# Performance work log

Measured on AMD Instinct MI355X. Metric: run time of the kernel, lower is better.

The kernel has to match this reference:

```python
import jax, jax.numpy as jnp
import numpy as np

B, D, H, K = 128, 512, 512, 16


def setup_inputs() -> dict:
    key = jax.random.key(0)
    ks = jax.random.split(key, 10)
    def xav(k, shape, fan_in, fan_out):
        # xavier_uniform per expert slice (same bound for all slices of the bank)
        bound = np.sqrt(6.0 / (fan_in + fan_out)).astype(np.float32)
        return jax.random.uniform(k, shape, jnp.float32, -bound, bound)
    u = jax.random.uniform(ks[9], (B, K), jnp.float32)
    u = u / jnp.sum(u, axis=-1, keepdims=True)  # soft convex selector
    return {
        "x_t": jax.random.normal(ks[0], (B, D), jnp.float32),
        "h_prev": jax.random.normal(ks[1], (B, H), jnp.float32),
        "u_t": u,
        "Wxr": xav(ks[2], (K, H, D), D, H),
        "Wxz": xav(ks[3], (K, H, D), D, H),
        "Wxn": xav(ks[4], (K, H, D), D, H),
        "Whr": xav(ks[5], (K, H, H), H, H),
        "Whz": xav(ks[6], (K, H, H), H, H),
        "Whn": xav(ks[7], (K, H, H), H, H),
        "bxr": jnp.zeros((K, H), jnp.float32),
        "bxz": jnp.zeros((K, H), jnp.float32),
        "bxn": jnp.zeros((K, H), jnp.float32),
        "brh": jnp.zeros((K, H), jnp.float32),
        "bzh": jnp.zeros((K, H), jnp.float32),
        "bnh": jnp.zeros((K, H), jnp.float32),
    }


def reference(x_t, h_prev, u_t, Wxr, Wxz, Wxn, Whr, Whz, Whn,
              bxr, bxz, bxn, brh, bzh, bnh):
    # mix biases: sum_k u[b,k] * b[k,h]
    mixb = lambda b: jnp.einsum('kh,bk->bh', b, u_t)
    # x-path: sum_k u[b,k] * (W[k] @ x[b]) + mixed bias; contracted without
    # materializing the [B,H,D] mixed weight (same math, better memory).
    def aff_x(W, b):
        return jnp.einsum('khd,bk,bd->bh', W, u_t, x_t, optimize=True) + mixb(b)
    # h-path: the original uses torch.einsum('bhh,bh->bh', W_mixed, h), which
    # extracts the DIAGONAL of the mixed [B,H,H] weight and multiplies
    # elementwise with h. Reproduce exactly via diagonals of the expert banks.
    def aff_h(W, b):
        dW = jnp.diagonal(W, axis1=1, axis2=2)  # [K, H]
        return jnp.einsum('kh,bk->bh', dW, u_t) * h_prev + mixb(b)
    r_t = jax.nn.sigmoid(aff_x(Wxr, bxr) + aff_h(Whr, brh))
    z_t = jax.nn.sigmoid(aff_x(Wxz, bxz) + aff_h(Whz, bzh))
    n_t = jnp.tanh(aff_x(Wxn, bxn) + r_t * aff_h(Whn, bnh))
    h_t = (1.0 - z_t) * n_t + z_t * h_prev
    return h_t
```

## Files before the change

kernel.cpp:

```cpp
#include <hip/hip_runtime.h>
#include <cstdint>
#include <cstddef>

#define Bb 128
#define Dd 512
#define Hh 512
#define KE 16

typedef unsigned short u16;
typedef unsigned int u32;
typedef __bf16 bf16x8 __attribute__((ext_vector_type(8)));
typedef float f32x4 __attribute__((ext_vector_type(4)));

union U8 { u16 h[8]; uint4 v; };

__device__ __forceinline__ u16 f2bf(float f) {
  u32 u = __float_as_uint(f);
  u32 r = (u + 0x7fffu + ((u >> 16) & 1u)) >> 16;
  return (u16)r;
}

__global__ __launch_bounds__(256) void prep_kernel(
    const float* __restrict__ x, const float* __restrict__ u,
    const float* __restrict__ Whr, const float* __restrict__ Whz,
    const float* __restrict__ Whn,
    u16* __restrict__ xu, float* __restrict__ yx, float* __restrict__ dW)
{
  int t = blockIdx.x * 256 + threadIdx.x;
  if (t < 131072) {
    int d8 = t & 63;
    int rest = t >> 6;
    int b = rest & 127;
    int k = rest >> 7;
    float uk = u[b * KE + k];
    const float4* xp = (const float4*)(x + b * Dd + d8 * 8);
    float4 x0 = xp[0], x1 = xp[1];
    U8 o;
    o.h[0] = f2bf(uk * x0.x); o.h[1] = f2bf(uk * x0.y);
    o.h[2] = f2bf(uk * x0.z); o.h[3] = f2bf(uk * x0.w);
    o.h[4] = f2bf(uk * x1.x); o.h[5] = f2bf(uk * x1.y);
    o.h[6] = f2bf(uk * x1.z); o.h[7] = f2bf(uk * x1.w);
    *(uint4*)(xu + ((k * Bb + b) * Dd + d8 * 8)) = o.v;
  } else if (t < 131072 + 49152) {
    int i = t - 131072;
    ((float4*)yx)[i] = make_float4(0.f, 0.f, 0.f, 0.f);
  } else if (t < 131072 + 49152 + 24576) {
    int i = t - (131072 + 49152);
    int h = i & 511;
    int k = (i >> 9) & 15;
    int bank = i >> 13;
    const float* Wp = bank == 0 ? Whr : (bank == 1 ? Whz : Whn);
    dW[i] = Wp[(size_t)k * Hh * Hh + h * (Hh + 1)];
  }
}

__global__ __launch_bounds__(256) void gemm_kernel(
    const float* __restrict__ Wxr, const float* __restrict__ Wxz,
    const float* __restrict__ Wxn,
    const u16* __restrict__ xu, float* __restrict__ yx)
{
  int bid = blockIdx.x;
  int k = bid & 15;
  int rem = bid >> 4;
  int bank = rem % 3;
  int ht = rem / 3;

  const float* Wsrc = (bank == 0 ? Wxr : (bank == 1 ? Wxz : Wxn));
  const float* Wp = Wsrc + (size_t)k * Hh * Dd + (size_t)ht * 128 * Dd;
  const u16* Ap = xu + k * Bb * Dd;
  float* yp = yx + bank * Bb * Hh;

  __shared__ __align__(16) u16 lA[2][128 * 64];
  __shared__ __align__(16) u16 lB[2][128 * 64];

  int tid = threadIdx.x;
  int lane = tid & 63;
  int wave = tid >> 6;
  int wm = wave >> 1;
  int wn = wave & 1;

  int ar = tid >> 1;
  int ac = (tid & 1) * 32;
  int br = tid >> 2;
  int bc = (tid & 3) * 16;

  uint4 aL[4];
  float4 bL[2][4];

  f32x4 acc[4][4];
#pragma unroll
  for (int i = 0; i < 4; ++i)
#pragma unroll
    for (int j = 0; j < 4; ++j) acc[i][j] = (f32x4){0.f, 0.f, 0.f, 0.f};

  auto LOAD = [&](int c) {
    int d0 = c * 64;
#pragma unroll
    for (int q = 0; q < 4; ++q)
      aL[q] = *(const uint4*)(Ap + ar * Dd + d0 + ac + 8 * q);
#pragma unroll
    for (int p = 0; p < 2; ++p)
#pragma unroll
      for (int q = 0; q < 4; ++q)
        bL[p][q] = *(const float4*)(Wp + (br + 64 * p) * Dd + d0 + bc + 4 * q);
  };

  auto STORE = [&](int nb) {
#pragma unroll
    for (int q = 0; q < 4; ++q) {
      int slot = ((ac >> 3) + q) ^ (ar & 7);
      *(uint4*)((char*)lA[nb] + ar * 128 + slot * 16) = aL[q];
    }
#pragma unroll
    for (int p = 0; p < 2; ++p) {
      int row = br + 64 * p;
      U8 g0, g1;
      g0.h[0] = f2bf(bL[p][0].x); g0.h[1] = f2bf(bL[p][0].y);
      g0.h[2] = f2bf(bL[p][0].z); g0.h[3] = f2bf(bL[p][0].w);
      g0.h[4] = f2bf(bL[p][1].x); g0.h[5] = f2bf(bL[p][1].y);
      g0.h[6] = f2bf(bL[p][1].z); g0.h[7] = f2bf(bL[p][1].w);
      g1.h[0] = f2bf(bL[p][2].x); g1.h[1] = f2bf(bL[p][2].y);
      g1.h[2] = f2bf(bL[p][2].z); g1.h[3] = f2bf(bL[p][2].w);
      g1.h[4] = f2bf(bL[p][3].x); g1.h[5] = f2bf(bL[p][3].y);
      g1.h[6] = f2bf(bL[p][3].z); g1.h[7] = f2bf(bL[p][3].w);
      int s0 = (bc >> 3) ^ (row & 7);
      int s1 = ((bc >> 3) + 1) ^ (row & 7);
      *(uint4*)((char*)lB[nb] + row * 128 + s0 * 16) = g0.v;
      *(uint4*)((char*)lB[nb] + row * 128 + s1 * 16) = g1.v;
    }
  };

  auto COMPUTE = [&](int cb) {
#pragma unroll
    for (int ks = 0; ks < 2; ++ks) {
      int kg = lane >> 4;
      int rlo = lane & 15;
      int slot = ks * 4 + kg;
      bf16x8 af[4], bfr[4];
#pragma unroll
      for (int fm = 0; fm < 4; ++fm) {
        int row = wm * 64 + fm * 16 + rlo;
        af[fm] = *(const bf16x8*)((char*)lA[cb] + row * 128 + ((slot ^ (row & 7)) * 16));
      }
#pragma unroll
      for (int fn = 0; fn < 4; ++fn) {
        int row = wn * 64 + fn * 16 + rlo;
        bfr[fn] = *(const bf16x8*)((char*)lB[cb] + row * 128 + ((slot ^ (row & 7)) * 16));
      }
#pragma unroll
      for (int fm = 0; fm < 4; ++fm)
#pragma unroll
        for (int fn = 0; fn < 4; ++fn)
          acc[fm][fn] = __builtin_amdgcn_mfma_f32_16x16x32_bf16(af[fm], bfr[fn],
                                                                acc[fm][fn], 0, 0, 0);
    }
  };

  LOAD(0);
  STORE(0);
  __syncthreads();
  for (int c = 0; c < 8; ++c) {
    int cb = c & 1, nb = cb ^ 1;
    if (c < 7) LOAD(c + 1);
    COMPUTE(cb);
    if (c < 7) STORE(nb);
    __syncthreads();
  }

  int rlo = lane & 15, rhi = lane >> 4;
#pragma unroll
  for (int fm = 0; fm < 4; ++fm)
#pragma unroll
    for (int fn = 0; fn < 4; ++fn)
#pragma unroll
      for (int j = 0; j < 4; ++j) {
        int b_ = wm * 64 + fm * 16 + rhi * 4 + j;
        int h_ = ht * 128 + wn * 64 + fn * 16 + rlo;
        unsafeAtomicAdd(&yp[b_ * Hh + h_], acc[fm][fn][j]);
      }
}

__global__ __launch_bounds__(256) void combine_kernel(
    const float* __restrict__ hprev, const float* __restrict__ u,
    const float* __restrict__ bxr, const float* __restrict__ bxz,
    const float* __restrict__ bxn, const float* __restrict__ brh,
    const float* __restrict__ bzh, const float* __restrict__ bnh,
    const float* __restrict__ yx, const float* __restrict__ dW,
    float* __restrict__ out)
{
  int b = blockIdx.x;
  __shared__ float su[KE];
  if (threadIdx.x < KE) su[threadIdx.x] = u[b * KE + threadIdx.x];
  __syncthreads();
  for (int h = threadIdx.x; h < Hh; h += 256) {
    float m_r = 0.f, m_z = 0.f, m_bxn = 0.f, m_bnh = 0.f;
    float d_r = 0.f, d_z = 0.f, d_n = 0.f;
#pragma unroll
    for (int k = 0; k < KE; ++k) {
      float uk = su[k];
      int i = k * Hh + h;
      m_r   += uk * (bxr[i] + brh[i]);
      m_z   += uk * (bxz[i] + bzh[i]);
      m_bxn += uk * bxn[i];
      m_bnh += uk * bnh[i];
      d_r   += uk * dW[0 * KE * Hh + i];
      d_z   += uk * dW[1 * KE * Hh + i];
      d_n   += uk * dW[2 * KE * Hh + i];
    }
    float hp = hprev[b * Hh + h];
    float pr = yx[0 * Bb * Hh + b * Hh + h] + m_r + d_r * hp;
    float pz = yx[1 * Bb * Hh + b * Hh + h] + m_z + d_z * hp;
    float r = 1.f / (1.f + expf(-pr));
    float z = 1.f / (1.f + expf(-pz));
    float pn = yx[2 * Bb * Hh + b * Hh + h] + m_bxn + r * (d_n * hp + m_bnh);
    float n = tanhf(pn);
    out[b * Hh + h] = (1.f - z) * n + z * hp;
  }
}

extern "C" void kernel_launch(void* const* d_in, const int* in_sizes, int n_in,
                              void* d_out, int out_size, void* d_ws, size_t ws_size,
                              hipStream_t stream) {
  const float* x   = (const float*)d_in[0];
  const float* hp  = (const float*)d_in[1];
  const float* u   = (const float*)d_in[2];
  const float* Wxr = (const float*)d_in[3];
  const float* Wxz = (const float*)d_in[4];
  const float* Wxn = (const float*)d_in[5];
  const float* Whr = (const float*)d_in[6];
  const float* Whz = (const float*)d_in[7];
  const float* Whn = (const float*)d_in[8];
  const float* bxr = (const float*)d_in[9];
  const float* bxz = (const float*)d_in[10];
  const float* bxn = (const float*)d_in[11];
  const float* brh = (const float*)d_in[12];
  const float* bzh = (const float*)d_in[13];
  const float* bnh = (const float*)d_in[14];
  float* out = (float*)d_out;

  u16* xu   = (u16*)d_ws;
  float* yx = (float*)((char*)d_ws + 2 * 1024 * 1024);
  float* dW = (float*)((char*)d_ws + 2 * 1024 * 1024 + 786432);

  prep_kernel<<<800, 256, 0, stream>>>(x, u, Whr, Whz, Whn, xu, yx, dW);
  gemm_kernel<<<192, 256, 0, stream>>>(Wxr, Wxz, Wxn, xu, yx);
  combine_kernel<<<128, 256, 0, stream>>>(hp, u, bxr, bxz, bxn, brh, bzh, bnh,
                                          yx, dW, out);
}
```

Before: 169.9 us.

## Fuse x*u scaling and diagonal extraction into GEMM, drop prep kernel

Removes the separate prep kernel. The GEMM now loads fp32 x directly, scales it by u[b,k] and converts to bf16 while staging into LDS, and also extracts the h-bank diagonals. Zeroing of the accumulation buffer moves to hipMemsetAsync. This avoids writing and rereading the 2 MB bf16 xu buffer and one kernel launch, at the cost of more global loads of x (fp32) per GEMM block and more registers per thread.

```diff
diff --git a/kernel.cpp b/kernel.cpp
--- a/kernel.cpp
+++ b/kernel.cpp
@@ -8,56 +8,18 @@
 #define KE 16
 
 typedef unsigned short u16;
-typedef unsigned int u32;
 typedef __bf16 bf16x8 __attribute__((ext_vector_type(8)));
 typedef float f32x4 __attribute__((ext_vector_type(4)));
 
-union U8 { u16 h[8]; uint4 v; };
-
-__device__ __forceinline__ u16 f2bf(float f) {
-  u32 u = __float_as_uint(f);
-  u32 r = (u + 0x7fffu + ((u >> 16) & 1u)) >> 16;
-  return (u16)r;
-}
-
-__global__ __launch_bounds__(256) void prep_kernel(
-    const float* __restrict__ x, const float* __restrict__ u,
-    const float* __restrict__ Whr, const float* __restrict__ Whz,
-    const float* __restrict__ Whn,
-    u16* __restrict__ xu, float* __restrict__ yx, float* __restrict__ dW)
-{
-  int t = blockIdx.x * 256 + threadIdx.x;
-  if (t < 131072) {
-    int d8 = t & 63;
-    int rest = t >> 6;
-    int b = rest & 127;
-    int k = rest >> 7;
-    float uk = u[b * KE + k];
-    const float4* xp = (const float4*)(x + b * Dd + d8 * 8);
-    float4 x0 = xp[0], x1 = xp[1];
-    U8 o;
-    o.h[0] = f2bf(uk * x0.x); o.h[1] = f2bf(uk * x0.y);
-    o.h[2] = f2bf(uk * x0.z); o.h[3] = f2bf(uk * x0.w);
-    o.h[4] = f2bf(uk * x1.x); o.h[5] = f2bf(uk * x1.y);
-    o.h[6] = f2bf(uk * x1.z); o.h[7] = f2bf(uk * x1.w);
-    *(uint4*)(xu + ((k * Bb + b) * Dd + d8 * 8)) = o.v;
-  } else if (t < 131072 + 49152) {
-    int i = t - 131072;
-    ((float4*)yx)[i] = make_float4(0.f, 0.f, 0.f, 0.f);
-  } else if (t < 131072 + 49152 + 24576) {
-    int i = t - (131072 + 49152);
-    int h = i & 511;
-    int k = (i >> 9) & 15;
-    int bank = i >> 13;
-    const float* Wp = bank == 0 ? Whr : (bank == 1 ? Whz : Whn);
-    dW[i] = Wp[(size_t)k * Hh * Hh + h * (Hh + 1)];
-  }
-}
+union U8 { __bf16 h[8]; uint4 v; };
 
 __global__ __launch_bounds__(256) void gemm_kernel(
     const float* __restrict__ Wxr, const float* __restrict__ Wxz,
     const float* __restrict__ Wxn,
-    const u16* __restrict__ xu, float* __restrict__ yx)
+    const float* __restrict__ Whr, const float* __restrict__ Whz,
+    const float* __restrict__ Whn,
+    const float* __restrict__ x, const float* __restrict__ u,
+    float* __restrict__ yx, float* __restrict__ dW)
 {
   int bid = blockIdx.x;
   int k = bid & 15;
@@ -65,27 +27,36 @@
   int bank = rem % 3;
   int ht = rem / 3;
 
-  const float* Wsrc = (bank == 0 ? Wxr : (bank == 1 ? Wxz : Wxn));
-  const float* Wp = Wsrc + (size_t)k * Hh * Dd + (size_t)ht * 128 * Dd;
-  const u16* Ap = xu + k * Bb * Dd;
+  const float* Wp = (bank == 0 ? Wxr : (bank == 1 ? Wxz : Wxn))
+                    + (size_t)k * Hh * Dd + (size_t)ht * 128 * Dd;
+  const float* Whp = (bank == 0 ? Whr : (bank == 1 ? Whz : Whn));
   float* yp = yx + bank * Bb * Hh;
+
+  int tid = threadIdx.x;
+
+  if (tid < 128) {
+    int h = ht * 128 + tid;
+    dW[(bank * KE + k) * Hh + h] =
+        Whp[(size_t)k * Hh * Hh + (size_t)h * (Hh + 1)];
+  }
 
   __shared__ __align__(16) u16 lA[2][128 * 64];
   __shared__ __align__(16) u16 lB[2][128 * 64];
 
-  int tid = threadIdx.x;
   int lane = tid & 63;
   int wave = tid >> 6;
   int wm = wave >> 1;
   int wn = wave & 1;
 
   int ar = tid >> 1;
-  int ac = (tid & 1) * 32;
+  int acf = (tid & 1) * 32;
   int br = tid >> 2;
-  int bc = (tid & 3) * 16;
-
-  uint4 aL[4];
-  float4 bL[2][4];
+  int bcf = (tid & 3) * 16;
+
+  float uk = u[ar * KE + k];
+
+  float4 aL[8];
+  float4 bL[8];
 
   f32x4 acc[4][4];
 #pragma unroll
@@ -96,63 +67,77 @@
   auto LOAD = [&](int c) {
     int d0 = c * 64;
 #pragma unroll
-    for (int q = 0; q < 4; ++q)
-      aL[q] = *(const uint4*)(Ap + ar * Dd + d0 + ac + 8 * q);
+    for (int q = 0; q < 8; ++q)
+      aL[q] = *(const float4*)(x + ar * Dd + d0 + acf + 4 * q);
 #pragma unroll
     for (int p = 0; p < 2; ++p)
 #pragma unroll
       for (int q = 0; q < 4; ++q)
-        bL[p][q] = *(const float4*)(Wp + (br + 64 * p) * Dd + d0 + bc + 4 * q);
+        bL[p * 4 + q] =
+            *(const float4*)(Wp + (br + 64 * p) * Dd + d0 + bcf + 4 * q);
   };
 
   auto STORE = [&](int nb) {
 #pragma unroll
     for (int q = 0; q < 4; ++q) {
-      int slot = ((ac >> 3) + q) ^ (ar & 7);
-      *(uint4*)((char*)lA[nb] + ar * 128 + slot * 16) = aL[q];
+      U8 o;
+      const float* f0 = (const float*)&aL[2 * q];
+      const float* f1 = (const float*)&aL[2 * q + 1];
+#pragma unroll
+      for (int j = 0; j < 4; ++j) {
+        o.h[j]     = (__bf16)(uk * f0[j]);
+        o.h[4 + j] = (__bf16)(uk * f1[j]);
+      }
+      int slot = ((acf >> 3) + q) ^ (ar & 7);
+      *(uint4*)((char*)lA[nb] + ar * 128 + slot * 16) = o.v;
     }
 #pragma unroll
     for (int p = 0; p < 2; ++p) {
       int row = br + 64 * p;
       U8 g0, g1;
-      g0.h[0] = f2bf(bL[p][0].x); g0.h[1] = f2bf(bL[p][0].y);
-      g0.h[2] = f2bf(bL[p][0].z); g0.h[3] = f2bf(bL[p][0].w);
-      g0.h[4] = f2bf(bL[p][1].x); g0.h[5] = f2bf(bL[p][1].y);
-      g0.h[6] = f2bf(bL[p][1].z); g0.h[7] = f2bf(bL[p][1].w);
-      g1.h[0] = f2bf(bL[p][2].x); g1.h[1] = f2bf(bL[p][2].y);
-      g1.h[2] = f2bf(bL[p][2].z); g1.h[3] = f2bf(bL[p][2].w);
-      g1.h[4] = f2bf(bL[p][3].x); g1.h[5] = f2bf(bL[p][3].y);
-      g1.h[6] = f2bf(bL[p][3].z); g1.h[7] = f2bf(bL[p][3].w);
-      int s0 = (bc >> 3) ^ (row & 7);
-      int s1 = ((bc >> 3) + 1) ^ (row & 7);
+      const float* c0 = (const float*)&bL[p * 4 + 0];
+      const float* c1 = (const float*)&bL[p * 4 + 1];
+      const float* c2 = (const float*)&bL[p * 4 + 2];
+      const float* c3 = (const float*)&bL[p * 4 + 3];
+#pragma unroll
+      for (int j = 0; j < 4; ++j) {
+        g0.h[j]     = (__bf16)c0[j];
+        g0.h[4 + j] = (__bf16)c1[j];
+        g1.h[j]     = (__bf16)c2[j];
+        g1.h[4 + j] = (__bf16)c3[j];
+      }
+      int s0 = (bcf >> 3) ^ (row & 7);
+      int s1 = ((bcf >> 3) + 1) ^ (row & 7);
       *(uint4*)((char*)lB[nb] + row * 128 + s0 * 16) = g0.v;
       *(uint4*)((char*)lB[nb] + row * 128 + s1 * 16) = g1.v;
     }
   };
 
   auto COMPUTE = [&](int cb) {
+    int kg = lane >> 4;
+    int rlo = lane & 15;
 #pragma unroll
     for (int ks = 0; ks < 2; ++ks) {
-      int kg = lane >> 4;
-      int rlo = lane & 15;
       int slot = ks * 4 + kg;
       bf16x8 af[4], bfr[4];
 #pragma unroll
       for (int fm = 0; fm < 4; ++fm) {
         int row = wm * 64 + fm * 16 + rlo;
-        af[fm] = *(const bf16x8*)((char*)lA[cb] + row * 128 + ((slot ^ (row & 7)) * 16));
+        af[fm] = *(const bf16x8*)((char*)lA[cb] + row * 128 +
+                                  ((slot ^ (row & 7)) * 16));
       }
 #pragma unroll
       for (int fn = 0; fn < 4; ++fn) {
         int row = wn * 64 + fn * 16 + rlo;
-        bfr[fn] = *(const bf16x8*)((char*)lB[cb] + row * 128 + ((slot ^ (row & 7)) * 16));
+        bfr[fn] = *(const bf16x8*)((char*)lB[cb] + row * 128 +
+                                   ((slot ^ (row & 7)) * 16));
       }
 #pragma unroll
       for (int fm = 0; fm < 4; ++fm)
 #pragma unroll
         for (int fn = 0; fn < 4; ++fn)
-          acc[fm][fn] = __builtin_amdgcn_mfma_f32_16x16x32_bf16(af[fm], bfr[fn],
-                                                                acc[fm][fn], 0, 0, 0);
+          acc[fm][fn] = __builtin_amdgcn_mfma_f32_16x16x32_bf16(
+              af[fm], bfr[fn], acc[fm][fn], 0, 0, 0);
     }
   };
 
@@ -238,12 +223,12 @@
   const float* bnh = (const float*)d_in[14];
   float* out = (float*)d_out;
 
-  u16* xu   = (u16*)d_ws;
-  float* yx = (float*)((char*)d_ws + 2 * 1024 * 1024);
-  float* dW = (float*)((char*)d_ws + 2 * 1024 * 1024 + 786432);
-
-  prep_kernel<<<800, 256, 0, stream>>>(x, u, Whr, Whz, Whn, xu, yx, dW);
-  gemm_kernel<<<192, 256, 0, stream>>>(Wxr, Wxz, Wxn, xu, yx);
+  float* yx = (float*)d_ws;
+  float* dW = (float*)((char*)d_ws + 786432);
+
+  hipMemsetAsync(yx, 0, 786432, stream);
+  gemm_kernel<<<192, 256, 0, stream>>>(Wxr, Wxz, Wxn, Whr, Whz, Whn,
+                                       x, u, yx, dW);
   combine_kernel<<<128, 256, 0, stream>>>(hp, u, bxr, bxz, bxn, brh, bzh, bnh,
                                           yx, dW, out);
 }
```

New measurement: 165.4 us. 1.03x faster.
